# Performance work log

Measured on AMD Instinct MI355X. Metric: run time of the kernel, lower is better.

Reference implementation:

```python
import jax, jax.numpy as jnp
import numpy as np
from jax import lax

B, T, D, R, V = 128, 8, 2048, 4, 512

def setup_inputs() -> dict:
    key = jax.random.key(0)
    k0, k1, k2, k3, k4 = jax.random.split(key, 5)
    # scales chosen so the TT products stay within fp32 range (see notes)
    input_embs = jax.random.normal(k0, (B, T, D), dtype=jnp.float32) * 0.1
    label_ids = jax.random.randint(k1, (B, T), 0, V)
    w_alpha = jax.random.normal(k2, (D, R), dtype=jnp.float32) * 0.04
    w_beta = jax.random.normal(k3, (D, R), dtype=jnp.float32) * 0.04
    w_vocab = jax.random.normal(k4, (D, V * R * R), dtype=jnp.float32) * 0.04
    return {"input_embs": input_embs, "label_ids": label_ids,
            "w_alpha": w_alpha, "w_beta": w_beta, "w_vocab": w_vocab}

def _tt_loss(input_embs, w_alpha, w_beta, w_vocab, label_ids):
    b, t, d = input_embs.shape
    flat = input_embs.reshape(-1, d)                    # [B*T, D]
    alpha = jnp.abs((flat @ w_alpha).reshape(b, t, R).mean(1))   # [B, R]
    beta = jnp.abs((flat @ w_beta).reshape(b, t, R).mean(1))     # [B, R]
    core = jnp.abs((flat @ w_vocab).reshape(b, t, R, V, R).mean(1))  # [B, R, V, R]

    # --- _select: gather per-position R x R cores and chain-multiply ---
    core_v = core.transpose(0, 2, 1, 3)                 # [B, V, R, R]
    sel = jnp.take_along_axis(core_v, label_ids[:, :, None, None], axis=1)  # [B, T, R, R]
    sel_t = jnp.swapaxes(sel, 0, 1)                     # [T, B, R, R]

    def chain(carry, m):
        return jnp.einsum('bik,bkj->bij', carry, m), None
    res, _ = lax.scan(chain, sel_t[0], sel_t[1:])       # [B, R, R]
    u = jnp.einsum('bi,bij,bj->b', alpha, res, beta)    # unnormalized probs [B]

    # --- normalization constant: marg^(T+1) contracted with alpha/beta ---
    marg = core.sum(2)                                  # [B, R, R]

    def pow_step(c, _):
        return jnp.einsum('bik,bkj->bij', c, marg), None
    zmat, _ = lax.scan(pow_step, marg, None, length=t)  # marg^(t+1)
    z = jnp.einsum('bi,bij,bj->b', alpha, zmat, beta)

    loss = -jnp.log(u / z)
    return loss.mean()

def reference(input_embs, label_ids, w_alpha, w_beta, w_vocab):
    return _tt_loss(input_embs, w_alpha, w_beta, w_vocab, label_ids)
```

## Files before the change

kernel.cpp:

```cpp
#include <hip/hip_runtime.h>
#include <math.h>

#define BB 128
#define TT 8
#define DD 2048
#define RR 4
#define VV 512

typedef __attribute__((ext_vector_type(8))) short short8;
typedef __attribute__((ext_vector_type(4))) float v4f;

__device__ __forceinline__ unsigned pack_bf16(float x, float y) {
    union { float f; unsigned u; } a, b;
    a.f = x; b.f = y;
    unsigned ua = a.u + 0x7fffu + ((a.u >> 16) & 1u);
    unsigned ub = b.u + 0x7fffu + ((b.u >> 16) & 1u);
    return (ua >> 16) | (ub & 0xffff0000u);
}

__global__ __launch_bounds__(256) void phaseA(const float* __restrict__ inp,
                                              const float* __restrict__ w_alpha,
                                              const float* __restrict__ w_beta,
                                              unsigned short* __restrict__ fmb,
                                              float* __restrict__ alphaA,
                                              float* __restrict__ betaA) {
    int bid = blockIdx.x;
    int b = bid >> 1, half = bid & 1;
    int tid = threadIdx.x;
    const float* base = inp + (size_t)b * TT * DD;
    float pa[4] = {0.f, 0.f, 0.f, 0.f};
    float pb[4] = {0.f, 0.f, 0.f, 0.f};
#pragma unroll
    for (int i = 0; i < 4; ++i) {
        int d = half * 1024 + i * 256 + tid;
        float s = 0.f;
#pragma unroll
        for (int t = 0; t < TT; ++t) s += base[t * DD + d];
        float v = s * (1.0f / TT);
        union { float f; unsigned u; } cv; cv.f = v;
        unsigned r = cv.u + 0x7fffu + ((cv.u >> 16) & 1u);
        fmb[b * DD + d] = (unsigned short)(r >> 16);
        float4 wa = *(const float4*)(w_alpha + d * 4);
        float4 wb = *(const float4*)(w_beta + d * 4);
        pa[0] += v * wa.x; pa[1] += v * wa.y; pa[2] += v * wa.z; pa[3] += v * wa.w;
        pb[0] += v * wb.x; pb[1] += v * wb.y; pb[2] += v * wb.z; pb[3] += v * wb.w;
    }
#pragma unroll
    for (int r = 0; r < 4; ++r) {
        for (int m = 1; m < 64; m <<= 1) {
            pa[r] += __shfl_xor(pa[r], m);
            pb[r] += __shfl_xor(pb[r], m);
        }
    }
    if ((tid & 63) == 0) {
#pragma unroll
        for (int r = 0; r < 4; ++r) {
            atomicAdd(&alphaA[b * 4 + r], pa[r]);
            atomicAdd(&betaA[b * 4 + r], pb[r]);
        }
    }
}

__global__ __launch_bounds__(512, 2) void phaseB(const unsigned short* __restrict__ fmb,
                                                 const float* __restrict__ wv,
                                                 const int* __restrict__ labels,
                                                 float* __restrict__ margA,
                                                 float* __restrict__ sel) {
    __shared__ unsigned short Ws[2][32][136];
    __shared__ int slab[BB * TT];

    const int tid = threadIdx.x;
    const int nb = blockIdx.x;
    const int col0 = nb * 32;

    slab[tid] = labels[tid];
    slab[tid + 512] = labels[tid + 512];

    const int nq = tid & 7;
    const int kp = tid >> 3;
    const int w = tid >> 6;
    const int lane = tid & 63;
    const int m15 = lane & 15;
    const int q = lane >> 4;

    const float* wbase = wv + (size_t)(2 * kp) * 8192 + col0 + nq * 4;
    const unsigned short* abase = fmb + (w * 16 + m15) * DD + q * 8;

    v4f acc0 = {0.f, 0.f, 0.f, 0.f};
    v4f acc1 = {0.f, 0.f, 0.f, 0.f};
    short8 afr[2][4];
    float4 sw0, sw1;

    sw0 = *(const float4*)(wbase);
    sw1 = *(const float4*)(wbase + 8192);
#pragma unroll
    for (int ks = 0; ks < 4; ++ks) afr[0][ks] = *(const short8*)(abase + ks * 32);
    {
        const float* f0 = (const float*)&sw0;
        const float* f1 = (const float*)&sw1;
#pragma unroll
        for (int j = 0; j < 4; ++j)
            *(unsigned*)&Ws[0][nq * 4 + j][2 * kp] = pack_bf16(f0[j], f1[j]);
    }
    __syncthreads();

    for (int c = 0; c < 16; ++c) {
        const int cur = c & 1;
        if (c < 15) {
            const float* wp = wbase + (size_t)(c + 1) * 128 * 8192;
            sw0 = *(const float4*)(wp);
            sw1 = *(const float4*)(wp + 8192);
            const unsigned short* ap = abase + (c + 1) * 128;
#pragma unroll
            for (int ks = 0; ks < 4; ++ks) afr[1 - cur][ks] = *(const short8*)(ap + ks * 32);
        }
#pragma unroll
        for (int ks = 0; ks < 4; ++ks) {
            short8 b0 = *(const short8*)&Ws[cur][m15][ks * 32 + q * 8];
            short8 b1 = *(const short8*)&Ws[cur][16 + m15][ks * 32 + q * 8];
            acc0 = __builtin_amdgcn_mfma_f32_16x16x32_bf16(afr[cur][ks], b0, acc0, 0, 0, 0);
            acc1 = __builtin_amdgcn_mfma_f32_16x16x32_bf16(afr[cur][ks], b1, acc1, 0, 0, 0);
        }
        if (c < 15) {
            const float* f0 = (const float*)&sw0;
            const float* f1 = (const float*)&sw1;
#pragma unroll
            for (int j = 0; j < 4; ++j)
                *(unsigned*)&Ws[1 - cur][nq * 4 + j][2 * kp] = pack_bf16(f0[j], f1[j]);
        }
        __syncthreads();
    }

    const int vbase = (nb & 63) * 8;
    const int iblk = nb >> 6;
    const int j = m15 & 3;
    const int v0 = vbase + (m15 >> 2);
    const float* a0p = (const float*)&acc0;
    const float* a1p = (const float*)&acc1;
#pragma unroll
    for (int r = 0; r < 4; ++r) {
        int m = w * 16 + q * 4 + r;
        float a0 = fabsf(a0p[r]);
        float a1 = fabsf(a1p[r]);
        float s = a0 + a1;
        s += __shfl_xor(s, 4);
        s += __shfl_xor(s, 8);
        if ((lane & 12) == 0) atomicAdd(&margA[m * 16 + iblk * 4 + j], s);
#pragma unroll
        for (int t = 0; t < TT; ++t) {
            int lv = slab[m * 8 + t];
            if (lv == v0)     sel[(m * 8 + t) * 16 + iblk * 4 + j] = a0;
            if (lv == v0 + 4) sel[(m * 8 + t) * 16 + iblk * 4 + j] = a1;
        }
    }
}

__global__ __launch_bounds__(128) void phaseD(const float* __restrict__ alpha,
                                              const float* __restrict__ beta,
                                              const float* __restrict__ marg,
                                              const float* __restrict__ sel,
                                              float* __restrict__ out) {
    int b = threadIdx.x;
    const float* sb = sel + b * TT * 16;
    float res[16], tmp[16], mm[16], zm[16];
#pragma unroll
    for (int e = 0; e < 16; ++e) res[e] = sb[e];
    for (int t = 1; t < TT; ++t) {
        const float* m = sb + t * 16;
#pragma unroll
        for (int i = 0; i < 4; ++i)
#pragma unroll
            for (int jj = 0; jj < 4; ++jj) {
                float s = 0.f;
#pragma unroll
                for (int k = 0; k < 4; ++k) s += res[i * 4 + k] * m[k * 4 + jj];
                tmp[i * 4 + jj] = s;
            }
#pragma unroll
        for (int e = 0; e < 16; ++e) res[e] = tmp[e];
    }
#pragma unroll
    for (int e = 0; e < 16; ++e) { mm[e] = marg[b * 16 + e]; zm[e] = mm[e]; }
    for (int st = 0; st < TT; ++st) {
#pragma unroll
        for (int i = 0; i < 4; ++i)
#pragma unroll
            for (int jj = 0; jj < 4; ++jj) {
                float s = 0.f;
#pragma unroll
                for (int k = 0; k < 4; ++k) s += zm[i * 4 + k] * mm[k * 4 + jj];
                tmp[i * 4 + jj] = s;
            }
#pragma unroll
        for (int e = 0; e < 16; ++e) zm[e] = tmp[e];
    }
    float u = 0.f, z = 0.f;
#pragma unroll
    for (int i = 0; i < 4; ++i) {
        float ai = fabsf(alpha[b * 4 + i]);
#pragma unroll
        for (int jj = 0; jj < 4; ++jj) {
            float bj = fabsf(beta[b * 4 + jj]);
            u += ai * res[i * 4 + jj] * bj;
            z += ai * zm[i * 4 + jj] * bj;
        }
    }
    float loss = logf(z) - logf(u);
    __shared__ float red[128];
    red[b] = loss;
    __syncthreads();
    for (int off = 64; off >= 1; off >>= 1) {
        if (b < off) red[b] += red[b + off];
        __syncthreads();
    }
    if (b == 0) out[0] = red[0] * (1.0f / BB);
}

extern "C" void kernel_launch(void* const* d_in, const int* in_sizes, int n_in,
                              void* d_out, int out_size, void* d_ws, size_t ws_size,
                              hipStream_t stream) {
    const float* inp     = (const float*)d_in[0];
    const int*   labels  = (const int*)d_in[1];
    const float* w_alpha = (const float*)d_in[2];
    const float* w_beta  = (const float*)d_in[3];
    const float* wv      = (const float*)d_in[4];
    float* out = (float*)d_out;

    float* ws    = (float*)d_ws;
    float* alpha = ws;
    float* beta  = ws + 512;
    float* marg  = ws + 1024;
    float* sel   = ws + 3072;
    unsigned short* fmb = (unsigned short*)(ws + 3072 + 16384);

    hipMemsetAsync(ws, 0, 3072 * sizeof(float), stream);

    phaseA<<<256, 256, 0, stream>>>(inp, w_alpha, w_beta, fmb, alpha, beta);
    phaseB<<<256, 512, 0, stream>>>(fmb, wv, labels, marg, sel);
    phaseD<<<1, 128, 0, stream>>>(alpha, beta, marg, sel, out);
}
```

Measured before the change: 128.3 us.

## Drop memset, write alpha/beta partials, split vocab GEMM into more smaller blocks

Removes the hipMemsetAsync by having phaseA block 0 zero the marg buffer and by writing per-half alpha/beta partial sums instead of atomics, which phaseD then adds. phaseB now uses 512 blocks of 256 threads, each covering 16 columns, with every wave computing two 16-row M tiles that share one B fragment. The main loop is fully unrolled and the final barrier is skipped. The aim is to cut launch and memset overhead and to spread the weight-streaming GEMM across more CUs. In exchange, each block does less reuse per B load.

```diff
diff --git a/kernel.cpp b/kernel.cpp
--- a/kernel.cpp
+++ b/kernel.cpp
@@ -22,11 +22,16 @@
                                               const float* __restrict__ w_alpha,
                                               const float* __restrict__ w_beta,
                                               unsigned short* __restrict__ fmb,
-                                              float* __restrict__ alphaA,
-                                              float* __restrict__ betaA) {
+                                              float* __restrict__ alphaP,
+                                              float* __restrict__ betaP,
+                                              float* __restrict__ marg) {
     int bid = blockIdx.x;
     int b = bid >> 1, half = bid & 1;
     int tid = threadIdx.x;
+    if (bid == 0) {
+#pragma unroll
+        for (int e = 0; e < 8; ++e) marg[e * 256 + tid] = 0.f;
+    }
     const float* base = inp + (size_t)b * TT * DD;
     float pa[4] = {0.f, 0.f, 0.f, 0.f};
     float pb[4] = {0.f, 0.f, 0.f, 0.f};
@@ -52,119 +57,141 @@
             pb[r] += __shfl_xor(pb[r], m);
         }
     }
+    __shared__ float red[4][8];
     if ((tid & 63) == 0) {
-#pragma unroll
-        for (int r = 0; r < 4; ++r) {
-            atomicAdd(&alphaA[b * 4 + r], pa[r]);
-            atomicAdd(&betaA[b * 4 + r], pb[r]);
-        }
-    }
-}
-
-__global__ __launch_bounds__(512, 2) void phaseB(const unsigned short* __restrict__ fmb,
+        int w = tid >> 6;
+#pragma unroll
+        for (int r = 0; r < 4; ++r) { red[w][r] = pa[r]; red[w][4 + r] = pb[r]; }
+    }
+    __syncthreads();
+    if (tid < 8) {
+        float s = red[0][tid] + red[1][tid] + red[2][tid] + red[3][tid];
+        if (tid < 4) alphaP[(half * BB + b) * 4 + tid] = s;
+        else         betaP[(half * BB + b) * 4 + (tid - 4)] = s;
+    }
+}
+
+__global__ __launch_bounds__(256, 4) void phaseB(const unsigned short* __restrict__ fmb,
                                                  const float* __restrict__ wv,
                                                  const int* __restrict__ labels,
-                                                 float* __restrict__ margA,
+                                                 float* __restrict__ marg,
                                                  float* __restrict__ sel) {
-    __shared__ unsigned short Ws[2][32][136];
+    __shared__ unsigned short Ws[2][16][136];
     __shared__ int slab[BB * TT];
 
     const int tid = threadIdx.x;
     const int nb = blockIdx.x;
-    const int col0 = nb * 32;
+    const int col0 = nb * 16;
+    const int iblk = nb >> 7;
+    const int c128 = nb & 127;
 
     slab[tid] = labels[tid];
+    slab[tid + 256] = labels[tid + 256];
     slab[tid + 512] = labels[tid + 512];
-
-    const int nq = tid & 7;
-    const int kp = tid >> 3;
+    slab[tid + 768] = labels[tid + 768];
+
+    const int c4 = tid & 3;
+    const int kp = tid >> 2;
     const int w = tid >> 6;
     const int lane = tid & 63;
     const int m15 = lane & 15;
     const int q = lane >> 4;
-
-    const float* wbase = wv + (size_t)(2 * kp) * 8192 + col0 + nq * 4;
-    const unsigned short* abase = fmb + (w * 16 + m15) * DD + q * 8;
+    const int row0 = w * 32;
+
+    const float* wbase = wv + (size_t)(2 * kp) * 8192 + col0 + c4 * 4;
+    const unsigned short* ab0 = fmb + (row0 + m15) * DD + q * 8;
+    const unsigned short* ab1 = ab0 + 16 * DD;
 
     v4f acc0 = {0.f, 0.f, 0.f, 0.f};
     v4f acc1 = {0.f, 0.f, 0.f, 0.f};
-    short8 afr[2][4];
+    short8 afr[2][2][4];
     float4 sw0, sw1;
 
     sw0 = *(const float4*)(wbase);
     sw1 = *(const float4*)(wbase + 8192);
 #pragma unroll
-    for (int ks = 0; ks < 4; ++ks) afr[0][ks] = *(const short8*)(abase + ks * 32);
+    for (int ks = 0; ks < 4; ++ks) {
+        afr[0][0][ks] = *(const short8*)(ab0 + ks * 32);
+        afr[0][1][ks] = *(const short8*)(ab1 + ks * 32);
+    }
     {
         const float* f0 = (const float*)&sw0;
         const float* f1 = (const float*)&sw1;
 #pragma unroll
-        for (int j = 0; j < 4; ++j)
-            *(unsigned*)&Ws[0][nq * 4 + j][2 * kp] = pack_bf16(f0[j], f1[j]);
+        for (int jj = 0; jj < 4; ++jj)
+            *(unsigned*)&Ws[0][c4 * 4 + jj][2 * kp] = pack_bf16(f0[jj], f1[jj]);
     }
     __syncthreads();
 
+#pragma unroll
     for (int c = 0; c < 16; ++c) {
         const int cur = c & 1;
         if (c < 15) {
             const float* wp = wbase + (size_t)(c + 1) * 128 * 8192;
             sw0 = *(const float4*)(wp);
             sw1 = *(const float4*)(wp + 8192);
-            const unsigned short* ap = abase + (c + 1) * 128;
-#pragma unroll
-            for (int ks = 0; ks < 4; ++ks) afr[1 - cur][ks] = *(const short8*)(ap + ks * 32);
+#pragma unroll
+            for (int ks = 0; ks < 4; ++ks) {
+                afr[1 - cur][0][ks] = *(const short8*)(ab0 + (c + 1) * 128 + ks * 32);
+                afr[1 - cur][1][ks] = *(const short8*)(ab1 + (c + 1) * 128 + ks * 32);
+            }
         }
 #pragma unroll
         for (int ks = 0; ks < 4; ++ks) {
-            short8 b0 = *(const short8*)&Ws[cur][m15][ks * 32 + q * 8];
-            short8 b1 = *(const short8*)&Ws[cur][16 + m15][ks * 32 + q * 8];
-            acc0 = __builtin_amdgcn_mfma_f32_16x16x32_bf16(afr[cur][ks], b0, acc0, 0, 0, 0);
-            acc1 = __builtin_amdgcn_mfma_f32_16x16x32_bf16(afr[cur][ks], b1, acc1, 0, 0, 0);
+            short8 bf = *(const short8*)&Ws[cur][m15][ks * 32 + q * 8];
+            acc0 = __builtin_amdgcn_mfma_f32_16x16x32_bf16(afr[cur][0][ks], bf, acc0, 0, 0, 0);
+            acc1 = __builtin_amdgcn_mfma_f32_16x16x32_bf16(afr[cur][1][ks], bf, acc1, 0, 0, 0);
         }
         if (c < 15) {
             const float* f0 = (const float*)&sw0;
             const float* f1 = (const float*)&sw1;
 #pragma unroll
-            for (int j = 0; j < 4; ++j)
-                *(unsigned*)&Ws[1 - cur][nq * 4 + j][2 * kp] = pack_bf16(f0[j], f1[j]);
-        }
-        __syncthreads();
-    }
-
-    const int vbase = (nb & 63) * 8;
-    const int iblk = nb >> 6;
-    const int j = m15 & 3;
-    const int v0 = vbase + (m15 >> 2);
+            for (int jj = 0; jj < 4; ++jj)
+                *(unsigned*)&Ws[1 - cur][c4 * 4 + jj][2 * kp] = pack_bf16(f0[jj], f1[jj]);
+            __syncthreads();
+        }
+    }
+
+    const int v0 = c128 * 4 + (m15 >> 2);
+    const int e = iblk * 4 + (m15 & 3);
     const float* a0p = (const float*)&acc0;
     const float* a1p = (const float*)&acc1;
 #pragma unroll
     for (int r = 0; r < 4; ++r) {
-        int m = w * 16 + q * 4 + r;
+        int ma = row0 + q * 4 + r;
+        int mb = ma + 16;
         float a0 = fabsf(a0p[r]);
         float a1 = fabsf(a1p[r]);
-        float s = a0 + a1;
-        s += __shfl_xor(s, 4);
-        s += __shfl_xor(s, 8);
-        if ((lane & 12) == 0) atomicAdd(&margA[m * 16 + iblk * 4 + j], s);
+        float s0 = a0 + __shfl_xor(a0, 4); s0 += __shfl_xor(s0, 8);
+        float s1 = a1 + __shfl_xor(a1, 4); s1 += __shfl_xor(s1, 8);
+        if (m15 < 4) {
+            atomicAdd(&marg[ma * 16 + e], s0);
+            atomicAdd(&marg[mb * 16 + e], s1);
+        }
 #pragma unroll
         for (int t = 0; t < TT; ++t) {
-            int lv = slab[m * 8 + t];
-            if (lv == v0)     sel[(m * 8 + t) * 16 + iblk * 4 + j] = a0;
-            if (lv == v0 + 4) sel[(m * 8 + t) * 16 + iblk * 4 + j] = a1;
-        }
-    }
-}
-
-__global__ __launch_bounds__(128) void phaseD(const float* __restrict__ alpha,
-                                              const float* __restrict__ beta,
+            if (slab[ma * 8 + t] == v0) sel[(ma * 8 + t) * 16 + e] = a0;
+            if (slab[mb * 8 + t] == v0) sel[(mb * 8 + t) * 16 + e] = a1;
+        }
+    }
+}
+
+__global__ __launch_bounds__(128) void phaseD(const float* __restrict__ alphaP,
+                                              const float* __restrict__ betaP,
                                               const float* __restrict__ marg,
                                               const float* __restrict__ sel,
                                               float* __restrict__ out) {
     int b = threadIdx.x;
+    float alpha[4], beta[4];
+#pragma unroll
+    for (int r = 0; r < 4; ++r) {
+        alpha[r] = fabsf(alphaP[b * 4 + r] + alphaP[512 + b * 4 + r]);
+        beta[r]  = fabsf(betaP[b * 4 + r] + betaP[512 + b * 4 + r]);
+    }
     const float* sb = sel + b * TT * 16;
     float res[16], tmp[16], mm[16], zm[16];
 #pragma unroll
-    for (int e = 0; e < 16; ++e) res[e] = sb[e];
+    for (int ee = 0; ee < 16; ++ee) res[ee] = sb[ee];
     for (int t = 1; t < TT; ++t) {
         const float* m = sb + t * 16;
 #pragma unroll
@@ -177,10 +204,10 @@
                 tmp[i * 4 + jj] = s;
             }
 #pragma unroll
-        for (int e = 0; e < 16; ++e) res[e] = tmp[e];
-    }
-#pragma unroll
-    for (int e = 0; e < 16; ++e) { mm[e] = marg[b * 16 + e]; zm[e] = mm[e]; }
+        for (int ee = 0; ee < 16; ++ee) res[ee] = tmp[ee];
+    }
+#pragma unroll
+    for (int ee = 0; ee < 16; ++ee) { mm[ee] = marg[b * 16 + ee]; zm[ee] = mm[ee]; }
     for (int st = 0; st < TT; ++st) {
 #pragma unroll
         for (int i = 0; i < 4; ++i)
@@ -192,17 +219,15 @@
                 tmp[i * 4 + jj] = s;
             }
 #pragma unroll
-        for (int e = 0; e < 16; ++e) zm[e] = tmp[e];
+        for (int ee = 0; ee < 16; ++ee) zm[ee] = tmp[ee];
     }
     float u = 0.f, z = 0.f;
 #pragma unroll
     for (int i = 0; i < 4; ++i) {
-        float ai = fabsf(alpha[b * 4 + i]);
 #pragma unroll
         for (int jj = 0; jj < 4; ++jj) {
-            float bj = fabsf(beta[b * 4 + jj]);
-            u += ai * res[i * 4 + jj] * bj;
-            z += ai * zm[i * 4 + jj] * bj;
+            u += alpha[i] * res[i * 4 + jj] * beta[jj];
+            z += alpha[i] * zm[i * 4 + jj] * beta[jj];
         }
     }
     float loss = logf(z) - logf(u);
@@ -226,16 +251,14 @@
     const float* wv      = (const float*)d_in[4];
     float* out = (float*)d_out;
 
-    float* ws    = (float*)d_ws;
-    float* alpha = ws;
-    float* beta  = ws + 512;
-    float* marg  = ws + 1024;
-    float* sel   = ws + 3072;
-    unsigned short* fmb = (unsigned short*)(ws + 3072 + 16384);
-
-    hipMemsetAsync(ws, 0, 3072 * sizeof(float), stream);
-
-    phaseA<<<256, 256, 0, stream>>>(inp, w_alpha, w_beta, fmb, alpha, beta);
-    phaseB<<<256, 512, 0, stream>>>(fmb, wv, labels, marg, sel);
-    phaseD<<<1, 128, 0, stream>>>(alpha, beta, marg, sel, out);
-}
+    float* ws     = (float*)d_ws;
+    float* alphaP = ws;
+    float* betaP  = ws + 1024;
+    float* marg   = ws + 2048;
+    float* sel    = ws + 4096;
+    unsigned short* fmb = (unsigned short*)(ws + 20480);
+
+    phaseA<<<256, 256, 0, stream>>>(inp, w_alpha, w_beta, fmb, alphaP, betaP, marg);
+    phaseB<<<512, 256, 0, stream>>>(fmb, wv, labels, marg, sel);
+    phaseD<<<1, 128, 0, stream>>>(alphaP, betaP, marg, sel, out);
+}
```

After: 146.3 us. +14.0%, slower.
